# Kernel tuning notes

Measured on AMD Instinct MI355X. Metric: run time of the kernel, lower is better.

Reference implementation:

```python
import jax, jax.numpy as jnp
import numpy as np

N = 100000
E = 1600000
F_IN, H1, H2, H3 = 128, 16, 64, 128


def setup_inputs() -> dict:
    key = jax.random.key(0)
    ks = jax.random.split(key, 10)
    x = jax.random.normal(ks[0], (N, F_IN), dtype=jnp.float32)
    edge_index = jax.random.randint(ks[1], (2, E), 0, N, dtype=jnp.int64)
    def lin(k, fi, fo):
        s = 1.0 / np.sqrt(fi)
        return jax.random.uniform(k, (fi, fo), jnp.float32, -s, s)
    W1 = lin(ks[2], F_IN, H1); b1 = jnp.zeros((H1,), jnp.float32)
    W2 = lin(ks[3], H1, H2);   b2 = jnp.zeros((H2,), jnp.float32)
    W3 = lin(ks[4], H2, H3);   b3 = jnp.zeros((H3,), jnp.float32)
    Wfc = lin(ks[5], H3, 1);   bfc = jnp.zeros((1,), jnp.float32)
    return {"x": x, "edge_index": edge_index, "W1": W1, "b1": b1,
            "W2": W2, "b2": b2, "W3": W3, "b3": b3, "Wfc": Wfc, "bfc": bfc}


def _build_graph(edge_index, n):
    # add self loops, compute symmetric normalization coefficients per edge
    loop = jnp.arange(n, dtype=edge_index.dtype)
    src = jnp.concatenate([edge_index[0], loop])
    dst = jnp.concatenate([edge_index[1], loop])
    deg = jax.ops.segment_sum(jnp.ones_like(dst, dtype=jnp.float32), dst, num_segments=n)
    dinv = jax.lax.rsqrt(deg)  # deg >= 1 due to self loops
    norm = dinv[src] * dinv[dst]  # [E+N]
    return src, dst, norm


def _gcn_conv(h, W, b, src, dst, norm, n):
    h = h @ W                       # [N, out]
    msg = h[src] * norm[:, None]    # gather + normalize, [E+N, out]
    return jax.ops.segment_sum(msg, dst, num_segments=n) + b


def reference(x, edge_index, W1, b1, W2, b2, W3, b3, Wfc, bfc):
    n = x.shape[0]
    src, dst, norm = _build_graph(edge_index, n)
    h = jax.nn.relu(_gcn_conv(x, W1, b1, src, dst, norm, n))
    h = jax.nn.relu(_gcn_conv(h, W2, b2, src, dst, norm, n))
    h = jax.nn.relu(_gcn_conv(h, W3, b3, src, dst, norm, n))
    return h @ Wfc + bfc  # [N, 1]
```

## Files before the change

### kernel.cpp

```cpp
#include <hip/hip_runtime.h>
#include <hip/hip_fp16.h>


#define NN 100000
#define NE 1600000
#define SHIFT 8
#define NB2 391
#define EPB 4096
#define NBLK 391
#define CHUNK 7

typedef _Float16 half8 __attribute__((ext_vector_type(8)));
typedef float f32x4 __attribute__((ext_vector_type(4)));

__device__ __forceinline__ float rdl_f(float v, int l) {
    return __int_as_float(__builtin_amdgcn_readlane(__float_as_int(v), l));
}

__device__ __forceinline__ void h2acc(unsigned u, float& a, float& b) {
    __half2 h = *reinterpret_cast<__half2*>(&u);
    float2 f = __half22float2(h);
    a += f.x; b += f.y;
}
__device__ __forceinline__ unsigned packh2(float a, float b) {
    __half2 h = __floats2half2_rn(a, b);
    return *reinterpret_cast<unsigned*>(&h);
}
__device__ __forceinline__ unsigned sc2(unsigned u, float s) {
    __half2 h = *reinterpret_cast<__half2*>(&u);
    float2 f = __half22float2(h);
    return packh2(f.x * s, f.y * s);
}

__global__ __launch_bounds__(256) void count_gemm1_k(const int* __restrict__ dst,
                                                     int* __restrict__ mat,
                                                     const float* __restrict__ x,
                                                     const float* __restrict__ W1,
                                                     __half* __restrict__ A, int n) {
    __shared__ int cnt[NB2];
    __shared__ unsigned sW2[64 * 16];
    __shared__ unsigned sIn2[16][66];
    const int tid = threadIdx.x;
    if ((int)blockIdx.x < NBLK) {
        for (int i = tid; i < NB2; i += 256) cnt[i] = 0;
        __syncthreads();
        const int e0 = blockIdx.x * EPB;
        const int e1 = min(e0 + EPB, NE);
        for (int i = e0 + tid; i < e1; i += 256) atomicAdd(&cnt[dst[i] >> SHIFT], 1);
        __syncthreads();
        for (int c = tid; c < NB2; c += 256) mat[blockIdx.x * NB2 + c] = cnt[c];
        return;
    }
    const int bid = blockIdx.x - NBLK;
    for (int i = tid; i < 64 * 16; i += 256) {
        const int k2 = i >> 4, m = i & 15;
        sW2[i] = packh2(W1[(2 * k2) * 16 + m], W1[(2 * k2 + 1) * 16 + m]);
    }
    const int row0 = bid * 16;
    const float4* in4 = (const float4*)x;
    for (int i = tid; i < 16 * 32; i += 256) {
        int r = i >> 5, kv = i & 31;
        int g = row0 + r;
        float4 v = make_float4(0.f, 0.f, 0.f, 0.f);
        if (g < n) v = in4[(long)g * 32 + kv];
        sIn2[r][kv * 2]     = packh2(v.x, v.y);
        sIn2[r][kv * 2 + 1] = packh2(v.z, v.w);
    }
    __syncthreads();
    const int r = tid >> 4, m = tid & 15;
    const int g = row0 + r;
    if (g < n) {
        float acc = 0.0f;
#pragma unroll
        for (int k2 = 0; k2 < 64; ++k2) {
            const __half2 a = *reinterpret_cast<const __half2*>(&sIn2[r][k2]);
            const __half2 w = *reinterpret_cast<const __half2*>(&sW2[k2 * 16 + m]);
            const float2 af = __half22float2(a);
            const float2 wf = __half22float2(w);
            acc = fmaf(af.x, wf.x, acc);
            acc = fmaf(af.y, wf.y, acc);
        }
        A[(long)g * 16 + m] = __float2half(acc);
    }
}

__global__ __launch_bounds__(64) void colscan_k(const int* __restrict__ mat,
                                                int* __restrict__ ofsT,
                                                int* __restrict__ colTotal) {
    const int c = blockIdx.x;
    const int lane = threadIdx.x;
    int v[CHUNK];
    int s = 0;
    const int base = lane * CHUNK;
#pragma unroll
    for (int j = 0; j < CHUNK; ++j) {
        int b = base + j;
        int x_ = (b < NBLK) ? mat[b * NB2 + c] : 0;
        v[j] = s;
        s += x_;
    }
    int inc = s;
#pragma unroll
    for (int d = 1; d < 64; d <<= 1) {
        int t = __shfl_up(inc, d, 64);
        if (lane >= d) inc += t;
    }
    const int excl = inc - s;
#pragma unroll
    for (int j = 0; j < CHUNK; ++j) {
        int b = base + j;
        if (b < NBLK) ofsT[b * NB2 + c] = excl + v[j];
    }
    if (lane == 63) colTotal[c] = excl + s;
}

__global__ __launch_bounds__(512) void p2_scatter_k(const int* __restrict__ src,
                                                    const int* __restrict__ dst,
                                                    const int* __restrict__ ofsT,
                                                    const int* __restrict__ colTotal,
                                                    unsigned* __restrict__ bucketed) {
    __shared__ int sc[512];
    __shared__ int cur[NB2];
    const int b = blockIdx.x;
    const int t = threadIdx.x;
    int v = (t < NB2) ? colTotal[t] : 0;
    sc[t] = v;
    __syncthreads();
    for (int off = 1; off < 512; off <<= 1) {
        int a = (t >= off) ? sc[t - off] : 0;
        __syncthreads();
        sc[t] += a;
        __syncthreads();
    }
    if (t < NB2) cur[t] = (sc[t] - v) + ofsT[b * NB2 + t];
    __syncthreads();
    const int e0 = b * EPB;
    const int e1 = min(e0 + EPB, NE);
    int i = e0 + t * 4;
    const int stride = 512 * 4;
    for (; i + 3 < e1; i += stride) {
        const int d0 = dst[i], d1 = dst[i + 1], d2 = dst[i + 2], d3 = dst[i + 3];
        const int s0 = src[i], s1 = src[i + 1], s2 = src[i + 2], s3 = src[i + 3];
        const int c0 = d0 >> SHIFT, c1 = d1 >> SHIFT;
        const int c2 = d2 >> SHIFT, c3 = d3 >> SHIFT;
        const int p0 = atomicAdd(&cur[c0], 1);
        const int p1 = atomicAdd(&cur[c1], 1);
        const int p2 = atomicAdd(&cur[c2], 1);
        const int p3 = atomicAdd(&cur[c3], 1);
        bucketed[p0] = ((unsigned)s0 << 8) | (unsigned)(d0 & 255);
        bucketed[p1] = ((unsigned)s1 << 8) | (unsigned)(d1 & 255);
        bucketed[p2] = ((unsigned)s2 << 8) | (unsigned)(d2 & 255);
        bucketed[p3] = ((unsigned)s3 << 8) | (unsigned)(d3 & 255);
    }
    for (; i < e1; ++i) {
        const int d = dst[i];
        const int c = d >> SHIFT;
        const int pos = atomicAdd(&cur[c], 1);
        bucketed[pos] = ((unsigned)src[i] << 8) | (unsigned)(d & 255);
    }
}

__global__ __launch_bounds__(512) void p3_csr_k(const unsigned* __restrict__ bucketed,
                                                const int* __restrict__ colTotal,
                                                int* __restrict__ rowptr,
                                                float* __restrict__ dinv,
                                                int* __restrict__ csr_src,
                                                __half* __restrict__ A) {
    __shared__ int sc[512];
    __shared__ int cnt[256];
    __shared__ int excl[256];
    __shared__ float ld[256];
    const int c = blockIdx.x;
    const int t = threadIdx.x;
    int v = (t < NB2) ? colTotal[t] : 0;
    sc[t] = v;
    if (t < 256) cnt[t] = 0;
    __syncthreads();
    for (int off = 1; off < 512; off <<= 1) {
        int a = (t >= off) ? sc[t - off] : 0;
        __syncthreads();
        sc[t] += a;
        __syncthreads();
    }
    const int end  = sc[c];
    const int base = (c > 0) ? sc[c - 1] : 0;
    for (int i = base + t; i < end; i += 512) atomicAdd(&cnt[bucketed[i] & 255u], 1);
    __syncthreads();
    if (t < 256) excl[t] = cnt[t];
    __syncthreads();
    for (int off = 1; off < 256; off <<= 1) {
        int a = (t < 256 && t >= off) ? excl[t - off] : 0;
        __syncthreads();
        if (t < 256) excl[t] += a;
        __syncthreads();
    }
    const int node0 = c << SHIFT;
    if (t < 256) {
        const int node = node0 + t;
        const int ex = excl[t] - cnt[t];
        if (node < NN) {
            rowptr[node] = base + ex;
            const float dv = rsqrtf((float)cnt[t] + 1.0f);
            dinv[node] = dv;
            ld[t] = dv;
        }
        excl[t] = ex;
    }
    if (c == NB2 - 1 && t == 0) rowptr[NN] = NE;
    __syncthreads();
    for (int i = base + t; i < end; i += 512) {
        const unsigned p = bucketed[i];
        const int pos = atomicAdd(&excl[p & 255u], 1);
        csr_src[base + pos] = (int)(p >> 8);
    }
    {
        const int node = node0 + (t >> 1);
        if (node < NN) {
            const float dv = ld[t >> 1];
            uint4* p = (uint4*)(A + (long)node * 16 + (t & 1) * 8);
            uint4 q = *p;
            q.x = sc2(q.x, dv); q.y = sc2(q.y, dv);
            q.z = sc2(q.z, dv); q.w = sc2(q.w, dv);
            *p = q;
        }
    }
}

__global__ __launch_bounds__(256) void gather16h_k(const int* __restrict__ rowptr,
                                                   const int* __restrict__ csr_src,
                                                   const float* __restrict__ dinv,
                                                   const __half* __restrict__ hs,
                                                   const float* __restrict__ bias,
                                                   __half* __restrict__ outp, int n) {
    const int lane = threadIdx.x & 63;
    const int wid0 = blockIdx.x * 4 + (threadIdx.x >> 6);
    const int nWaves = gridDim.x * 4;
    const int q = lane & 3;
    const int sub = lane >> 2;
    const uint2* h2p = (const uint2*)hs;
    const float4 b = ((const float4*)bias)[q];
    for (int g = wid0; g < n; g += nWaves) {
        const float dg = dinv[g];
        const int beg = rowptr[g], end = rowptr[g + 1];
        float a0 = 0.f, a1 = 0.f, a2 = 0.f, a3 = 0.f;
        if (sub == 0) {
            uint2 v = h2p[(long)g * 4 + q];
            h2acc(v.x, a0, a1); h2acc(v.y, a2, a3);
        }
        for (int j0 = beg; j0 < end; j0 += 16) {
            int idx = j0 + sub;
            if (idx < end) {
                const int s = csr_src[idx];
                uint2 v = h2p[(long)s * 4 + q];
                h2acc(v.x, a0, a1); h2acc(v.y, a2, a3);
            }
        }
#pragma unroll
        for (int m = 4; m <= 32; m <<= 1) {
            a0 += __shfl_xor(a0, m, 64);
            a1 += __shfl_xor(a1, m, 64);
            a2 += __shfl_xor(a2, m, 64);
            a3 += __shfl_xor(a3, m, 64);
        }
        if (sub == 0) {
            float v0 = fmaxf(fmaf(dg, a0, b.x), 0.0f) * dg;
            float v1 = fmaxf(fmaf(dg, a1, b.y), 0.0f) * dg;
            float v2 = fmaxf(fmaf(dg, a2, b.z), 0.0f) * dg;
            float v3 = fmaxf(fmaf(dg, a3, b.w), 0.0f) * dg;
            uint2 w;
            w.x = packh2(v0, v1);
            w.y = packh2(v2, v3);
            ((uint2*)outp)[(long)g * 4 + q] = w;
        }
    }
}

__global__ __launch_bounds__(256) void g16gemm2h_k(const int* __restrict__ rowptr,
                                                   const int* __restrict__ csr_src,
                                                   const float* __restrict__ dinv,
                                                   const __half* __restrict__ hs,
                                                   const float* __restrict__ W2,
                                                   const float* __restrict__ b2,
                                                   __half* __restrict__ outp, int n) {
    const int lane = threadIdx.x & 63;
    const int wid = blockIdx.x * 4 + (threadIdx.x >> 6);
    const int nWaves = gridDim.x * 4;
    float w2[16];
#pragma unroll
    for (int k = 0; k < 16; ++k) w2[k] = W2[k * 64 + lane];
    const float bm = b2[lane];
    const int q = lane & 3;
    const int sub = lane >> 2;
    const uint2* h2p = (const uint2*)hs;
    for (int g = wid; g < n; g += nWaves) {
        const float dg = dinv[g];
        const int beg = rowptr[g], end = rowptr[g + 1];
        float a0 = 0.f, a1 = 0.f, a2 = 0.f, a3 = 0.f;
        if (sub == 0) {
            uint2 v = h2p[(long)g * 4 + q];
            h2acc(v.x, a0, a1); h2acc(v.y, a2, a3);
        }
        for (int j0 = beg; j0 < end; j0 += 16) {
            int idx = j0 + sub;
            if (idx < end) {
                const int s = csr_src[idx];
                uint2 v = h2p[(long)s * 4 + q];
                h2acc(v.x, a0, a1); h2acc(v.y, a2, a3);
            }
        }
#pragma unroll
        for (int m = 4; m <= 32; m <<= 1) {
            a0 += __shfl_xor(a0, m, 64);
            a1 += __shfl_xor(a1, m, 64);
            a2 += __shfl_xor(a2, m, 64);
            a3 += __shfl_xor(a3, m, 64);
        }
        float t = 0.0f;
#pragma unroll
        for (int ql = 0; ql < 4; ++ql) {
            t = fmaf(rdl_f(a0, ql), w2[4 * ql + 0], t);
            t = fmaf(rdl_f(a1, ql), w2[4 * ql + 1], t);
            t = fmaf(rdl_f(a2, ql), w2[4 * ql + 2], t);
            t = fmaf(rdl_f(a3, ql), w2[4 * ql + 3], t);
        }
        float r = fmaxf(fmaf(dg, t, bm), 0.0f);
        outp[(long)g * 64 + lane] = __float2half(r * dg);
    }
}

__global__ __launch_bounds__(256) void gather64h_k(const int* __restrict__ rowptr,
                                                   const int* __restrict__ csr_src,
                                                   const float* __restrict__ dinv,
                                                   const __half* __restrict__ hs,
                                                   __half* __restrict__ outp, int n) {
    const int g = (blockIdx.x * 256 + threadIdx.x) >> 6;
    if (g >= n) return;
    const int lane = threadIdx.x & 63;
    const int q = lane & 7;
    const int sub = lane >> 3;
    const float dg = dinv[g];
    const int beg = rowptr[g], end = rowptr[g + 1];
    const uint4* h4 = (const uint4*)hs;
    float a[8];
#pragma unroll
    for (int i = 0; i < 8; ++i) a[i] = 0.f;
    if (sub == 0) {
        uint4 v = h4[(long)g * 8 + q];
        h2acc(v.x, a[0], a[1]); h2acc(v.y, a[2], a[3]);
        h2acc(v.z, a[4], a[5]); h2acc(v.w, a[6], a[7]);
    }
    int j0 = beg;
    for (; j0 + 16 <= end; j0 += 16) {
        const int s0 = csr_src[j0 + sub];
        const int s1 = csr_src[j0 + 8 + sub];
        const uint4 v0 = h4[(long)s0 * 8 + q];
        const uint4 v1 = h4[(long)s1 * 8 + q];
        h2acc(v0.x, a[0], a[1]); h2acc(v0.y, a[2], a[3]);
        h2acc(v0.z, a[4], a[5]); h2acc(v0.w, a[6], a[7]);
        h2acc(v1.x, a[0], a[1]); h2acc(v1.y, a[2], a[3]);
        h2acc(v1.z, a[4], a[5]); h2acc(v1.w, a[6], a[7]);
    }
    for (; j0 < end; j0 += 8) {
        int idx = j0 + sub;
        if (idx < end) {
            const int s = csr_src[idx];
            const uint4 v = h4[(long)s * 8 + q];
            h2acc(v.x, a[0], a[1]); h2acc(v.y, a[2], a[3]);
            h2acc(v.z, a[4], a[5]); h2acc(v.w, a[6], a[7]);
        }
    }
#pragma unroll
    for (int m = 8; m <= 32; m <<= 1) {
#pragma unroll
        for (int i = 0; i < 8; ++i) a[i] += __shfl_xor(a[i], m, 64);
    }
    if (sub == 0) {
        uint4 w;
        w.x = packh2(a[0] * dg, a[1] * dg);
        w.y = packh2(a[2] * dg, a[3] * dg);
        w.z = packh2(a[4] * dg, a[5] * dg);
        w.w = packh2(a[6] * dg, a[7] * dg);
        ((uint4*)outp)[(long)g * 8 + q] = w;
    }
}

__global__ __launch_bounds__(256) void head_mfma_k(const __half* __restrict__ agg,
                                                   const float* __restrict__ W3,
                                                   const float* __restrict__ b3,
                                                   const float* __restrict__ Wfc,
                                                   const float* __restrict__ bfc,
                                                   float* __restrict__ out, int n) {
    __shared__ _Float16 sWf[8192];
    const int tid = threadIdx.x;
    for (int i = tid; i < 8192; i += 256) {
        const int j = i & 7;
        const int l = (i >> 3) & 63;
        const int th = i >> 9;
        const int k = (th & 1) * 32 + ((l >> 4) << 3) + j;
        const int nn = (th >> 1) * 16 + (l & 15);
        sWf[i] = (_Float16)W3[k * 128 + nn];
    }
    __syncthreads();
    const int lane = tid & 63;
    const int wid = blockIdx.x * 4 + (tid >> 6);
    const int nWaves = gridDim.x * 4;
    const int col = lane & 15;
    const int kg = lane >> 4;
    half8 wf[16];
#pragma unroll
    for (int q2 = 0; q2 < 16; ++q2)
        wf[q2] = *((const half8*)&sWf[(q2 * 64 + lane) * 8]);
    float b3v[8], wfv[8];
#pragma unroll
    for (int t = 0; t < 8; ++t) {
        b3v[t] = b3[t * 16 + col];
        wfv[t] = Wfc[t * 16 + col];
    }
    const float bb = bfc[0];
    const int nTiles = n >> 4;
    union { uint4 u; half8 h; } cva, cvb;
    for (int tile = wid; tile < nTiles; tile += nWaves) {
        const int node0 = tile << 4;
        const uint4* rowp = (const uint4*)(agg + (long)(node0 + col) * 64);
        cva.u = rowp[kg];
        cvb.u = rowp[4 + kg];
        const half8 a0 = cva.h, a1 = cvb.h;
        f32x4 c[8];
#pragma unroll
        for (int t = 0; t < 8; ++t) {
            f32x4 z = {0.f, 0.f, 0.f, 0.f};
            c[t] = __builtin_amdgcn_mfma_f32_16x16x32_f16(a0, wf[t * 2], z, 0, 0, 0);
            c[t] = __builtin_amdgcn_mfma_f32_16x16x32_f16(a1, wf[t * 2 + 1], c[t], 0, 0, 0);
        }
        float s0 = 0.f, s1 = 0.f, s2 = 0.f, s3 = 0.f;
#pragma unroll
        for (int t = 0; t < 8; ++t) {
            s0 += fmaxf(c[t][0] + b3v[t], 0.f) * wfv[t];
            s1 += fmaxf(c[t][1] + b3v[t], 0.f) * wfv[t];
            s2 += fmaxf(c[t][2] + b3v[t], 0.f) * wfv[t];
            s3 += fmaxf(c[t][3] + b3v[t], 0.f) * wfv[t];
        }
#pragma unroll
        for (int m = 1; m <= 8; m <<= 1) {
            s0 += __shfl_xor(s0, m, 64);
            s1 += __shfl_xor(s1, m, 64);
            s2 += __shfl_xor(s2, m, 64);
            s3 += __shfl_xor(s3, m, 64);
        }
        if (col == 0) {
            const int nb = node0 + kg * 4;
            out[nb]     = s0 + bb;
            out[nb + 1] = s1 + bb;
            out[nb + 2] = s2 + bb;
            out[nb + 3] = s3 + bb;
        }
    }
}

extern "C" void kernel_launch(void* const* d_in, const int* in_sizes, int n_in,
                              void* d_out, int out_size, void* d_ws, size_t ws_size,
                              hipStream_t stream) {
    const float* x    = (const float*)d_in[0];
    const int*   ei   = (const int*)d_in[1];
    const float* W1   = (const float*)d_in[2];
    const float* b1   = (const float*)d_in[3];
    const float* W2   = (const float*)d_in[4];
    const float* b2   = (const float*)d_in[5];
    const float* W3   = (const float*)d_in[6];
    const float* b3   = (const float*)d_in[7];
    const float* Wfc  = (const float*)d_in[8];
    const float* bfc  = (const float*)d_in[9];
    float* out = (float*)d_out;

    const int* src = ei;
    const int* dst = ei + NE;

    float* dinv        = (float*)d_ws;
    int*   rowptr      = (int*)(dinv + NN);
    int*   mat         = rowptr + NN + 8;
    int*   ofsT        = mat + NBLK * NB2 + 4;
    int*   colTotal    = ofsT + NBLK * NB2 + 4;
    int*   csr_src     = colTotal + 512;
    unsigned* bucketed = (unsigned*)(csr_src + NE + 64);
    __half* A_h        = (__half*)(bucketed + NE);
    __half* B_h        = A_h + (long)NN * 16;
    __half* C_h        = B_h + (long)NN * 16;
    __half* agg_h      = C_h + (long)NN * 64;

    const int T = 256;

    const int gemmBlocks = (NN + 15) / 16;
    count_gemm1_k<<<NBLK + gemmBlocks, T, 0, stream>>>(dst, mat, x, W1, A_h, NN);
    colscan_k<<<NB2, 64, 0, stream>>>(mat, ofsT, colTotal);
    p2_scatter_k<<<NBLK, 512, 0, stream>>>(src, dst, ofsT, colTotal, bucketed);
    p3_csr_k<<<NB2, 512, 0, stream>>>(bucketed, colTotal, rowptr, dinv, csr_src, A_h);

    gather16h_k<<<3072, T, 0, stream>>>(rowptr, csr_src, dinv, A_h, b1, B_h, NN);
    g16gemm2h_k<<<3072, T, 0, stream>>>(rowptr, csr_src, dinv, B_h, W2, b2, C_h, NN);
    gather64h_k<<<(NN + 3) / 4, T, 0, stream>>>(rowptr, csr_src, dinv, C_h, agg_h, NN);
    head_mfma_k<<<256, T, 0, stream>>>(agg_h, W3, b3, Wfc, bfc, out, NN);
}
```

Before: 268.8 us.

## Use MFMA for first-layer GEMM and precompute bucket bases in scatter

```diff
diff --git a/kernel.cpp b/kernel.cpp
--- a/kernel.cpp
+++ b/kernel.cpp
@@ -38,8 +38,8 @@
                                                      const float* __restrict__ W1,
                                                      __half* __restrict__ A, int n) {
     __shared__ int cnt[NB2];
-    __shared__ unsigned sW2[64 * 16];
-    __shared__ unsigned sIn2[16][66];
+    __shared__ _Float16 sW1f[2048];
+    __shared__ unsigned sxu[4][16][68];
     const int tid = threadIdx.x;
     if ((int)blockIdx.x < NBLK) {
         for (int i = tid; i < NB2; i += 256) cnt[i] = 0;
@@ -52,35 +52,38 @@
         return;
     }
     const int bid = blockIdx.x - NBLK;
-    for (int i = tid; i < 64 * 16; i += 256) {
-        const int k2 = i >> 4, m = i & 15;
-        sW2[i] = packh2(W1[(2 * k2) * 16 + m], W1[(2 * k2 + 1) * 16 + m]);
-    }
-    const int row0 = bid * 16;
+    const int row0 = bid * 64;
+    for (int i = tid; i < 2048; i += 256) {
+        const int kt = i >> 9;
+        const int l = (i >> 3) & 63;
+        const int j = i & 7;
+        const int k = kt * 32 + ((l >> 4) << 3) + j;
+        sW1f[i] = (_Float16)W1[k * 16 + (l & 15)];
+    }
     const float4* in4 = (const float4*)x;
-    for (int i = tid; i < 16 * 32; i += 256) {
-        int r = i >> 5, kv = i & 31;
-        int g = row0 + r;
+    for (int i = tid; i < 2048; i += 256) {
+        const int r = i >> 5, kv = i & 31;
+        const int g = row0 + r;
         float4 v = make_float4(0.f, 0.f, 0.f, 0.f);
         if (g < n) v = in4[(long)g * 32 + kv];
-        sIn2[r][kv * 2]     = packh2(v.x, v.y);
-        sIn2[r][kv * 2 + 1] = packh2(v.z, v.w);
-    }
-    __syncthreads();
-    const int r = tid >> 4, m = tid & 15;
-    const int g = row0 + r;
-    if (g < n) {
-        float acc = 0.0f;
-#pragma unroll
-        for (int k2 = 0; k2 < 64; ++k2) {
-            const __half2 a = *reinterpret_cast<const __half2*>(&sIn2[r][k2]);
-            const __half2 w = *reinterpret_cast<const __half2*>(&sW2[k2 * 16 + m]);
-            const float2 af = __half22float2(a);
-            const float2 wf = __half22float2(w);
-            acc = fmaf(af.x, wf.x, acc);
-            acc = fmaf(af.y, wf.y, acc);
-        }
-        A[(long)g * 16 + m] = __float2half(acc);
+        unsigned* su = &sxu[r >> 4][r & 15][0];
+        su[kv * 2]     = packh2(v.x, v.y);
+        su[kv * 2 + 1] = packh2(v.z, v.w);
+    }
+    __syncthreads();
+    const int w = tid >> 6, l = tid & 63;
+    const int node0 = row0 + w * 16;
+    f32x4 c = {0.f, 0.f, 0.f, 0.f};
+#pragma unroll
+    for (int kt = 0; kt < 4; ++kt) {
+        const half8 a = *(const half8*)&sxu[w][l & 15][kt * 16 + ((l >> 4) << 2)];
+        const half8 b = *(const half8*)&sW1f[kt * 512 + l * 8];
+        c = __builtin_amdgcn_mfma_f32_16x16x32_f16(a, b, c, 0, 0, 0);
+    }
+#pragma unroll
+    for (int i = 0; i < 4; ++i) {
+        const int g = node0 + ((l >> 4) << 2) + i;
+        if (g < n) A[(long)g * 16 + (l & 15)] = __float2half(c[i]);
     }
 }
 
@@ -118,6 +121,7 @@
                                                     const int* __restrict__ dst,
                                                     const int* __restrict__ ofsT,
                                                     const int* __restrict__ colTotal,
+                                                    int* __restrict__ bucketBase,
                                                     unsigned* __restrict__ bucketed) {
     __shared__ int sc[512];
     __shared__ int cur[NB2];
@@ -133,6 +137,10 @@
         __syncthreads();
     }
     if (t < NB2) cur[t] = (sc[t] - v) + ofsT[b * NB2 + t];
+    if (b == 0) {
+        if (t < NB2) bucketBase[t] = sc[t] - v;
+        if (t == NB2) bucketBase[NB2] = NE;
+    }
     __syncthreads();
     const int e0 = b * EPB;
     const int e1 = min(e0 + EPB, NE);
@@ -161,29 +169,20 @@
 }
 
 __global__ __launch_bounds__(512) void p3_csr_k(const unsigned* __restrict__ bucketed,
-                                                const int* __restrict__ colTotal,
+                                                const int* __restrict__ bucketBase,
                                                 int* __restrict__ rowptr,
                                                 float* __restrict__ dinv,
                                                 int* __restrict__ csr_src,
                                                 __half* __restrict__ A) {
-    __shared__ int sc[512];
     __shared__ int cnt[256];
     __shared__ int excl[256];
     __shared__ float ld[256];
     const int c = blockIdx.x;
     const int t = threadIdx.x;
-    int v = (t < NB2) ? colTotal[t] : 0;
-    sc[t] = v;
+    const int base = bucketBase[c];
+    const int end  = bucketBase[c + 1];
     if (t < 256) cnt[t] = 0;
     __syncthreads();
-    for (int off = 1; off < 512; off <<= 1) {
-        int a = (t >= off) ? sc[t - off] : 0;
-        __syncthreads();
-        sc[t] += a;
-        __syncthreads();
-    }
-    const int end  = sc[c];
-    const int base = (c > 0) ? sc[c - 1] : 0;
     for (int i = base + t; i < end; i += 512) atomicAdd(&cnt[bucketed[i] & 255u], 1);
     __syncthreads();
     if (t < 256) excl[t] = cnt[t];
@@ -480,7 +479,8 @@
     int*   mat         = rowptr + NN + 8;
     int*   ofsT        = mat + NBLK * NB2 + 4;
     int*   colTotal    = ofsT + NBLK * NB2 + 4;
-    int*   csr_src     = colTotal + 512;
+    int*   bucketBase  = colTotal + 512;
+    int*   csr_src     = bucketBase + 512;
     unsigned* bucketed = (unsigned*)(csr_src + NE + 64);
     __half* A_h        = (__half*)(bucketed + NE);
     __half* B_h        = A_h + (long)NN * 16;
@@ -489,11 +489,11 @@
 
     const int T = 256;
 
-    const int gemmBlocks = (NN + 15) / 16;
+    const int gemmBlocks = (NN + 63) / 64;
     count_gemm1_k<<<NBLK + gemmBlocks, T, 0, stream>>>(dst, mat, x, W1, A_h, NN);
     colscan_k<<<NB2, 64, 0, stream>>>(mat, ofsT, colTotal);
-    p2_scatter_k<<<NBLK, 512, 0, stream>>>(src, dst, ofsT, colTotal, bucketed);
-    p3_csr_k<<<NB2, 512, 0, stream>>>(bucketed, colTotal, rowptr, dinv, csr_src, A_h);
+    p2_scatter_k<<<NBLK, 512, 0, stream>>>(src, dst, ofsT, colTotal, bucketBase, bucketed);
+    p3_csr_k<<<NB2, 512, 0, stream>>>(bucketed, bucketBase, rowptr, dinv, csr_src, A_h);
 
     gather16h_k<<<3072, T, 0, stream>>>(rowptr, csr_src, dinv, A_h, b1, B_h, NN);
     g16gemm2h_k<<<3072, T, 0, stream>>>(rowptr, csr_src, dinv, B_h, W2, b2, C_h, NN);
```

Result: no change. 265.8 us (-1.1%).
